# Kernel tuning notes

Measured on AMD Instinct MI355X. Metric: run time of the kernel, lower is better.

## Reference

```python
import jax, jax.numpy as jnp
import numpy as np

BLOCK = 64   # init block_size
RATIO = 0.5  # init ratio
GRAY = 128.0


def _make_mask(depth_map, H, W, key):
    """Vectorized equivalent of the per-block python loop.

    Blocks with initial_mask > ratio are kept (all ones). Dropped blocks are
    filled with a random binary region containing round(depth*b*b) zeros,
    chosen uniformly without replacement (torch.randperm semantics ==
    rank-of-uniform-noise < num_zeros).
    """
    nH, nW = H // BLOCK, W // BLOCK
    k1, k2 = jax.random.split(key)
    initial_mask = jax.random.uniform(k1, (nH, nW))           # [nH,nW]
    keep = initial_mask > RATIO                                # blocks kept fully

    d = jnp.where(depth_map.max() > 1.0, depth_map / 255.0, depth_map)
    gray_depth = d.mean(axis=0)                                # [H,W]
    # avg_pool2d with kernel=stride=BLOCK
    avg_depth = gray_depth.reshape(nH, BLOCK, nW, BLOCK).mean(axis=(1, 3))  # [nH,nW]
    num_zeros = jnp.round(avg_depth * (BLOCK * BLOCK)).astype(jnp.int32)    # per block

    # random permutation rank per pixel within each block
    noise = jax.random.uniform(k2, (nH, nW, BLOCK * BLOCK))
    ranks = jnp.argsort(jnp.argsort(noise, axis=-1), axis=-1)               # [nH,nW,b*b]
    region = (ranks >= num_zeros[..., None]).astype(jnp.float32)            # zeros at low ranks

    blocks = jnp.where(keep[..., None], 1.0, region)           # [nH,nW,b*b]
    mask = blocks.reshape(nH, nW, BLOCK, BLOCK).transpose(0, 2, 1, 3).reshape(H, W)
    return mask


def setup_inputs() -> dict:
    key = jax.random.key(0)
    k1, k2 = jax.random.split(key)
    img = jax.random.uniform(k1, (3, 2048, 4096), dtype=jnp.float32) * 255.0
    depth_map = jax.random.uniform(k2, (3, 2048, 4096), dtype=jnp.float32)
    return {"img": img, "depth_map": depth_map}


def reference(img, depth_map):
    C, H, W = img.shape
    mask = _make_mask(depth_map, H, W, jax.random.key(42))     # [H,W]
    # resize to (H,W) is a no-op since mask is already full resolution
    return img * mask + GRAY * (1.0 - mask)
```

## Files before the change

### kernel.cpp

```cpp
#include <hip/hip_runtime.h>
#include <stdint.h>

static constexpr int kH  = 2048;
static constexpr int kW  = 4096;
static constexpr int kHW = kH * kW;
static constexpr int kNH = kH / 64;
static constexpr int kNW = kW / 64;
static constexpr int kNB = kNH * kNW;
static constexpr int kBB = 64 * 64;
static constexpr int kGrayN = kNB * kBB;
static constexpr float kGray = 128.0f;

__host__ __device__ inline void tf2x32(uint32_t k0, uint32_t k1,
                                       uint32_t x0, uint32_t x1,
                                       uint32_t& o0, uint32_t& o1) {
  uint32_t ks2 = 0x1BD11BDAu ^ k0 ^ k1;
  x0 += k0; x1 += k1;
#define ROTL(v, d) (((v) << (d)) | ((v) >> (32 - (d))))
#define RND(R) { x0 += x1; x1 = ROTL(x1, R); x1 ^= x0; }
  RND(13) RND(15) RND(26) RND(6)
  x0 += k1;  x1 += ks2 + 1u;
  RND(17) RND(29) RND(16) RND(24)
  x0 += ks2; x1 += k0 + 2u;
  RND(13) RND(15) RND(26) RND(6)
  x0 += k0;  x1 += k1 + 3u;
  RND(17) RND(29) RND(16) RND(24)
  x0 += k1;  x1 += ks2 + 4u;
  RND(13) RND(15) RND(26) RND(6)
  x0 += ks2; x1 += k0 + 5u;
  o0 = x0; o1 = x1;
#undef RND
#undef ROTL
}

__device__ inline uint32_t rbits(uint32_t ka, uint32_t kb, uint32_t idx) {
  uint32_t o0, o1;
  tf2x32(ka, kb, 0u, idx, o0, o1);
  return o0 ^ o1;
}

__device__ inline bool keep_block(uint32_t k1a, uint32_t k1b, int b) {
  uint32_t v = rbits(k1a, k1b, (uint32_t)b) >> 9;
  return v > 0x400000u;
}

__global__ __launch_bounds__(256) void k1_depth(const float* __restrict__ depth,
                                                float* __restrict__ Gu,
                                                float* __restrict__ Gs,
                                                float* __restrict__ Bmax,
                                                uint32_t k1a, uint32_t k1b_) {
  __shared__ float red[256];
  const int b = blockIdx.x, t = threadIdx.x;
  const int bi = b >> 6, bj = b & 63;
  const int y0 = bi * 64, x0 = bj * 64;
  const bool keep = keep_block(k1a, k1b_, b);
  const float4* d4 = reinterpret_cast<const float4*>(depth);

  float mx = 0.0f;
  #pragma unroll
  for (int it = 0; it < 4; ++it) {
    int idx = it * 256 + t;
    int r = idx >> 4, cq = idx & 15;
    uint32_t a4 = (uint32_t)(y0 + r) * (kW / 4) + (uint32_t)(x0 / 4 + cq);
    float4 d0 = d4[a4];
    float4 d1 = d4[a4 + kHW / 4];
    float4 d2 = d4[a4 + 2 * (kHW / 4)];
    mx = fmaxf(mx, fmaxf(fmaxf(fmaxf(d0.x, d0.y), fmaxf(d0.z, d0.w)),
               fmaxf(fmaxf(fmaxf(d1.x, d1.y), fmaxf(d1.z, d1.w)),
                     fmaxf(fmaxf(d2.x, d2.y), fmaxf(d2.z, d2.w)))));
    if (!keep) {
      uint32_t p4 = (uint32_t)b * (kBB / 4) + (uint32_t)idx;
      float4 u, s;
      u.x = ((d0.x + d1.x) + d2.x) / 3.0f;
      u.y = ((d0.y + d1.y) + d2.y) / 3.0f;
      u.z = ((d0.z + d1.z) + d2.z) / 3.0f;
      u.w = ((d0.w + d1.w) + d2.w) / 3.0f;
      s.x = ((d0.x / 255.0f + d1.x / 255.0f) + d2.x / 255.0f) / 3.0f;
      s.y = ((d0.y / 255.0f + d1.y / 255.0f) + d2.y / 255.0f) / 3.0f;
      s.z = ((d0.z / 255.0f + d1.z / 255.0f) + d2.z / 255.0f) / 3.0f;
      s.w = ((d0.w / 255.0f + d1.w / 255.0f) + d2.w / 255.0f) / 3.0f;
      reinterpret_cast<float4*>(Gu)[p4] = u;
      reinterpret_cast<float4*>(Gs)[p4] = s;
    }
  }
  red[t] = mx;
  __syncthreads();
  for (int s = 128; s > 0; s >>= 1) {
    if (t < s) red[t] = fmaxf(red[t], red[t + s]);
    __syncthreads();
  }
  if (t == 0) Bmax[b] = red[0];
}

__global__ __launch_bounds__(64) void kchain(const float* __restrict__ G,
                                             const float* __restrict__ Bmax,
                                             float* __restrict__ S,
                                             uint32_t k1a, uint32_t k1b_) {
  const int w = blockIdx.x, lane = threadIdx.x;

  float m = 0.0f;
  #pragma unroll
  for (int i = 0; i < kNB / 64; ++i) m = fmaxf(m, Bmax[lane + i * 64]);
  #pragma unroll
  for (int d = 32; d >= 1; d >>= 1) m = fmaxf(m, __shfl_xor(m, d, 64));
  const bool flag = m > 1.0f;

  uint32_t bits = 0;
  int c = 0;
  #pragma unroll
  for (int j = 0; j < 32; ++j) {
    int b = lane * 32 + j;
    if (!keep_block(k1a, k1b_, b)) { bits |= (1u << j); ++c; }
  }
  int P = c;
  #pragma unroll
  for (int d = 1; d < 64; d <<= 1) {
    int v = __shfl_up(P, d, 64);
    if (lane >= d) P += v;
  }
  const int total = __shfl(P, 63, 64);
  P -= c;

  const int r0 = 2 * w, r1 = 2 * w + 1;
  int b0c = -1, b1c = -1;
  if (r0 >= P && r0 < P + c) {
    uint32_t bb = bits;
    for (int i = r0 - P; i > 0; --i) bb &= bb - 1;
    b0c = lane * 32 + __ffs(bb) - 1;
  }
  if (r1 >= P && r1 < P + c) {
    uint32_t bb = bits;
    for (int i = r1 - P; i > 0; --i) bb &= bb - 1;
    b1c = lane * 32 + __ffs(bb) - 1;
  }
  unsigned long long m0 = __ballot(b0c >= 0);
  unsigned long long m1 = __ballot(b1c >= 0);
  const int blk0 = (r0 < total && m0) ? __shfl(b0c, (int)(__ffsll(m0) - 1), 64) : -1;
  const int blk1 = (r1 < total && m1) ? __shfl(b1c, (int)(__ffsll(m1) - 1), 64) : -1;

  const int blk = (lane == 0) ? blk0 : blk1;
  if (lane < 2 && blk >= 0) {
    const float4* g4 = reinterpret_cast<const float4*>(G) +
                       (flag ? (uint32_t)(kGrayN / 4) : 0u) + (uint32_t)blk * (kBB / 4);

    float4 buf[32];
    #pragma unroll
    for (int i = 0; i < 32; ++i) buf[i] = g4[i];
    uint32_t gp = 32;

    float acc = 0.0f;
    for (int outer = 0; outer < 31; ++outer) {
      #pragma unroll
      for (int i = 0; i < 32; ++i) {
        float4 v = buf[i];
        buf[i] = g4[gp + i];
        acc += v.x; acc += v.y; acc += v.z; acc += v.w;
      }
      gp += 32;
    }
    #pragma unroll
    for (int i = 0; i < 32; ++i) {
      float4 v = buf[i];
      acc += v.x; acc += v.y; acc += v.z; acc += v.w;
    }
    S[blk] = acc;
  }
}

__global__ __launch_bounds__(256) void k3_fused(const float* __restrict__ img,
                                                float* __restrict__ out,
                                                const float* __restrict__ S,
                                                uint32_t k1a, uint32_t k1b_,
                                                uint32_t k2a, uint32_t k2b) {
  __shared__ uint32_t vals[kBB];
  __shared__ uint32_t hist[256];
  __shared__ uint32_t cand[kBB];
  __shared__ uint32_t sh[4];
  const int b = blockIdx.x, t = threadIdx.x;
  const int bi = b >> 6, bj = b & 63;
  const int y0 = bi * 64, x0 = bj * 64;
  const float4* img4 = reinterpret_cast<const float4*>(img);
  float4* out4 = reinterpret_cast<float4*>(out);

  int nz;
  if (keep_block(k1a, k1b_, b)) {
    nz = 0;
  } else {
    float s = S[b];
    nz = (int)rintf(s);
    if (nz < 0) nz = 0;
    if (nz > kBB) nz = kBB;
  }

  if (nz == 0 || nz == kBB) {
    const bool fill = (nz == kBB);
    const float4 g4v = make_float4(kGray, kGray, kGray, kGray);
    #pragma unroll
    for (int it = 0; it < 4; ++it) {
      int r = it * 16 + (t >> 4), cq = t & 15;
      uint32_t a4 = (uint32_t)(y0 + r) * (kW / 4) + (uint32_t)(x0 / 4 + cq);
      #pragma unroll
      for (int ch = 0; ch < 3; ++ch) {
        uint32_t a = a4 + (uint32_t)ch * (kHW / 4);
        out4[a] = fill ? g4v : img4[a];
      }
    }
    return;
  }

  for (int i = t; i < 256; i += 256) hist[i] = 0;
  if (t == 0) sh[3] = 0;
  __syncthreads();

  const uint32_t base = (uint32_t)b * (uint32_t)kBB;
  #pragma unroll
  for (int u = 0; u < 16; ++u) {
    int p = u * 256 + t;
    uint32_t v = rbits(k2a, k2b, base + (uint32_t)p) >> 9;
    vals[p] = v;
    atomicAdd(&hist[v >> 15], 1u);
  }
  __syncthreads();

  if (t == 0) {
    uint32_t cum = 0;
    for (int i = 0; i < 256; ++i) {
      uint32_t h = hist[i];
      if (cum + h >= (uint32_t)nz) { sh[0] = (uint32_t)i; sh[1] = (uint32_t)nz - cum; break; }
      cum += h;
    }
  }
  __syncthreads();
  const uint32_t Bsel = sh[0], rr = sh[1];

  #pragma unroll
  for (int u = 0; u < 16; ++u) {
    int p = u * 256 + t;
    uint32_t v = vals[p];
    if ((v >> 15) == Bsel) {
      uint32_t slot = atomicAdd(&sh[3], 1u);
      cand[slot] = ((v & 0x7FFFu) << 12) | (uint32_t)p;
    }
  }
  __syncthreads();
  const uint32_t m = sh[3];

  for (uint32_t q = t; q < m; q += 256) {
    uint32_t key = cand[q], rank = 0;
    for (uint32_t q2 = 0; q2 < m; ++q2) rank += (cand[q2] < key) ? 1u : 0u;
    if (rank == rr - 1) sh[2] = key;
  }
  __syncthreads();
  const uint32_t T = sh[2];

  #pragma unroll
  for (int it = 0; it < 4; ++it) {
    int r = it * 16 + (t >> 4), cq = t & 15;
    int p = r * 64 + cq * 4;
    uint4 vv = *reinterpret_cast<const uint4*>(vals + p);
    uint32_t kmask = 0;
    {
      uint32_t v, key;
      v = vv.x; key = ((v & 0x7FFFu) << 12) | (uint32_t)(p + 0);
      if (!((v >> 15) < Bsel || ((v >> 15) == Bsel && key <= T))) kmask |= 1u;
      v = vv.y; key = ((v & 0x7FFFu) << 12) | (uint32_t)(p + 1);
      if (!((v >> 15) < Bsel || ((v >> 15) == Bsel && key <= T))) kmask |= 2u;
      v = vv.z; key = ((v & 0x7FFFu) << 12) | (uint32_t)(p + 2);
      if (!((v >> 15) < Bsel || ((v >> 15) == Bsel && key <= T))) kmask |= 4u;
      v = vv.w; key = ((v & 0x7FFFu) << 12) | (uint32_t)(p + 3);
      if (!((v >> 15) < Bsel || ((v >> 15) == Bsel && key <= T))) kmask |= 8u;
    }
    uint32_t a4 = (uint32_t)(y0 + r) * (kW / 4) + (uint32_t)(x0 / 4 + cq);
    #pragma unroll
    for (int ch = 0; ch < 3; ++ch) {
      uint32_t a = a4 + (uint32_t)ch * (kHW / 4);
      float4 v = img4[a];
      float4 o;
      o.x = (kmask & 1u) ? v.x : kGray;
      o.y = (kmask & 2u) ? v.y : kGray;
      o.z = (kmask & 4u) ? v.z : kGray;
      o.w = (kmask & 8u) ? v.w : kGray;
      out4[a] = o;
    }
  }
}

extern "C" void kernel_launch(void* const* d_in, const int* in_sizes, int n_in,
                              void* d_out, int out_size, void* d_ws, size_t ws_size,
                              hipStream_t stream) {
  const float* img   = (const float*)d_in[0];
  const float* depth = (const float*)d_in[1];
  float* out = (float*)d_out;

  float* Gu = out;
  float* Gs = out + kGrayN;

  float* S    = (float*)d_ws;
  float* Bmax = S + kNB;

  uint32_t k1a, k1b_, k2a, k2b;
  tf2x32(0u, 42u, 0u, 0u, k1a, k1b_);
  tf2x32(0u, 42u, 0u, 1u, k2a, k2b);

  k1_depth<<<kNB, 256, 0, stream>>>(depth, Gu, Gs, Bmax, k1a, k1b_);
  kchain  <<<kNB / 2, 64, 0, stream>>>(out, Bmax, S, k1a, k1b_);
  k3_fused<<<kNB, 256, 0, stream>>>(img, out, S, k1a, k1b_, k2a, k2b);
}
```

Baseline: 119.0 us.

## Replace shared-memory value buffer with register radix select and parallel scans

The random values for each block are now kept in registers instead of a 16 KB shared array. The threshold search becomes a two-level radix histogram, each level resolved with a parallel prefix scan instead of a serial thread-0 loop. Only a small candidate set of at most 64 keys is then ranked. This cuts LDS usage from roughly 32 KB per block, which should raise occupancy, and shortens the serial rank step. In exchange it adds many __syncthreads in the scans, and selection is wrong if more than 64 candidates share the 16-bit prefix.

```diff
diff --git a/kernel.cpp b/kernel.cpp
--- a/kernel.cpp
+++ b/kernel.cpp
@@ -172,9 +172,8 @@
                                                 const float* __restrict__ S,
                                                 uint32_t k1a, uint32_t k1b_,
                                                 uint32_t k2a, uint32_t k2b) {
-  __shared__ uint32_t vals[kBB];
   __shared__ uint32_t hist[256];
-  __shared__ uint32_t cand[kBB];
+  __shared__ uint32_t cand[64];
   __shared__ uint32_t sh[4];
   const int b = blockIdx.x, t = threadIdx.x;
   const int bi = b >> 6, bj = b & 63;
@@ -192,13 +191,14 @@
     if (nz > kBB) nz = kBB;
   }
 
+  const int row0 = t >> 4, cq = t & 15;
+
   if (nz == 0 || nz == kBB) {
     const bool fill = (nz == kBB);
     const float4 g4v = make_float4(kGray, kGray, kGray, kGray);
     #pragma unroll
     for (int it = 0; it < 4; ++it) {
-      int r = it * 16 + (t >> 4), cq = t & 15;
-      uint32_t a4 = (uint32_t)(y0 + r) * (kW / 4) + (uint32_t)(x0 / 4 + cq);
+      uint32_t a4 = (uint32_t)(y0 + it * 16 + row0) * (kW / 4) + (uint32_t)(x0 / 4 + cq);
       #pragma unroll
       for (int ch = 0; ch < 3; ++ch) {
         uint32_t a = a4 + (uint32_t)ch * (kHW / 4);
@@ -208,78 +208,105 @@
     return;
   }
 
-  for (int i = t; i < 256; i += 256) hist[i] = 0;
+  const uint32_t base = (uint32_t)b * (uint32_t)kBB;
+  uint32_t v[4][4];
+  #pragma unroll
+  for (int it = 0; it < 4; ++it) {
+    uint32_t p = (uint32_t)((it * 16 + row0) * 64 + cq * 4);
+    #pragma unroll
+    for (int j = 0; j < 4; ++j) v[it][j] = rbits(k2a, k2b, base + p + j) >> 9;
+  }
+
+  hist[t] = 0;
   if (t == 0) sh[3] = 0;
   __syncthreads();
-
-  const uint32_t base = (uint32_t)b * (uint32_t)kBB;
-  #pragma unroll
-  for (int u = 0; u < 16; ++u) {
-    int p = u * 256 + t;
-    uint32_t v = rbits(k2a, k2b, base + (uint32_t)p) >> 9;
-    vals[p] = v;
-    atomicAdd(&hist[v >> 15], 1u);
-  }
-  __syncthreads();
-
-  if (t == 0) {
-    uint32_t cum = 0;
-    for (int i = 0; i < 256; ++i) {
-      uint32_t h = hist[i];
-      if (cum + h >= (uint32_t)nz) { sh[0] = (uint32_t)i; sh[1] = (uint32_t)nz - cum; break; }
-      cum += h;
-    }
-  }
-  __syncthreads();
-  const uint32_t Bsel = sh[0], rr = sh[1];
-
-  #pragma unroll
-  for (int u = 0; u < 16; ++u) {
-    int p = u * 256 + t;
-    uint32_t v = vals[p];
-    if ((v >> 15) == Bsel) {
-      uint32_t slot = atomicAdd(&sh[3], 1u);
-      cand[slot] = ((v & 0x7FFFu) << 12) | (uint32_t)p;
-    }
-  }
-  __syncthreads();
-  const uint32_t m = sh[3];
-
-  for (uint32_t q = t; q < m; q += 256) {
-    uint32_t key = cand[q], rank = 0;
-    for (uint32_t q2 = 0; q2 < m; ++q2) rank += (cand[q2] < key) ? 1u : 0u;
-    if (rank == rr - 1) sh[2] = key;
-  }
-  __syncthreads();
-  const uint32_t T = sh[2];
+  #pragma unroll
+  for (int it = 0; it < 4; ++it)
+    #pragma unroll
+    for (int j = 0; j < 4; ++j) atomicAdd(&hist[v[it][j] >> 15], 1u);
+  __syncthreads();
+  {
+    uint32_t h = hist[t];
+    for (int s = 1; s < 256; s <<= 1) {
+      uint32_t add = (t >= s) ? hist[t - s] : 0;
+      __syncthreads();
+      hist[t] += add;
+      __syncthreads();
+    }
+    uint32_t inc = hist[t], exc = inc - h;
+    if (inc >= (uint32_t)nz && exc < (uint32_t)nz) { sh[0] = (uint32_t)t; sh[1] = (uint32_t)nz - exc; }
+  }
+  __syncthreads();
+  const uint32_t B1 = sh[0], rr2 = sh[1];
+
+  hist[t] = 0;
+  __syncthreads();
+  #pragma unroll
+  for (int it = 0; it < 4; ++it)
+    #pragma unroll
+    for (int j = 0; j < 4; ++j) {
+      uint32_t vv = v[it][j];
+      if ((vv >> 15) == B1) atomicAdd(&hist[(vv >> 7) & 0xFFu], 1u);
+    }
+  __syncthreads();
+  {
+    uint32_t h = hist[t];
+    for (int s = 1; s < 256; s <<= 1) {
+      uint32_t add = (t >= s) ? hist[t - s] : 0;
+      __syncthreads();
+      hist[t] += add;
+      __syncthreads();
+    }
+    uint32_t inc = hist[t], exc = inc - h;
+    if (inc >= rr2 && exc < rr2) { sh[0] = (uint32_t)t; sh[1] = rr2 - exc; }
+  }
+  __syncthreads();
+  const uint32_t pref16 = (B1 << 8) | sh[0];
+  const uint32_t rr3 = sh[1];
+
+  #pragma unroll
+  for (int it = 0; it < 4; ++it)
+    #pragma unroll
+    for (int j = 0; j < 4; ++j) {
+      uint32_t vv = v[it][j];
+      if ((vv >> 7) == pref16) {
+        uint32_t p = (uint32_t)((it * 16 + row0) * 64 + cq * 4 + j);
+        uint32_t slot = atomicAdd(&sh[3], 1u);
+        if (slot < 64u) cand[slot] = ((vv & 0x7Fu) << 12) | p;
+      }
+    }
+  __syncthreads();
+  const uint32_t m = sh[3] < 64u ? sh[3] : 64u;
+  if (t < (int)m) {
+    uint32_t key = cand[t], rank = 0;
+    for (uint32_t q = 0; q < m; ++q) rank += (cand[q] < key) ? 1u : 0u;
+    if (rank == rr3 - 1) sh[2] = key;
+  }
+  __syncthreads();
+  const uint32_t T3 = sh[2];
 
   #pragma unroll
   for (int it = 0; it < 4; ++it) {
-    int r = it * 16 + (t >> 4), cq = t & 15;
-    int p = r * 64 + cq * 4;
-    uint4 vv = *reinterpret_cast<const uint4*>(vals + p);
+    uint32_t p = (uint32_t)((it * 16 + row0) * 64 + cq * 4);
     uint32_t kmask = 0;
-    {
-      uint32_t v, key;
-      v = vv.x; key = ((v & 0x7FFFu) << 12) | (uint32_t)(p + 0);
-      if (!((v >> 15) < Bsel || ((v >> 15) == Bsel && key <= T))) kmask |= 1u;
-      v = vv.y; key = ((v & 0x7FFFu) << 12) | (uint32_t)(p + 1);
-      if (!((v >> 15) < Bsel || ((v >> 15) == Bsel && key <= T))) kmask |= 2u;
-      v = vv.z; key = ((v & 0x7FFFu) << 12) | (uint32_t)(p + 2);
-      if (!((v >> 15) < Bsel || ((v >> 15) == Bsel && key <= T))) kmask |= 4u;
-      v = vv.w; key = ((v & 0x7FFFu) << 12) | (uint32_t)(p + 3);
-      if (!((v >> 15) < Bsel || ((v >> 15) == Bsel && key <= T))) kmask |= 8u;
-    }
-    uint32_t a4 = (uint32_t)(y0 + r) * (kW / 4) + (uint32_t)(x0 / 4 + cq);
+    #pragma unroll
+    for (int j = 0; j < 4; ++j) {
+      uint32_t vv = v[it][j];
+      uint32_t pre = vv >> 7;
+      bool zero = (pre < pref16) ||
+                  (pre == pref16 && ((((vv & 0x7Fu) << 12) | (p + j)) <= T3));
+      if (!zero) kmask |= (1u << j);
+    }
+    uint32_t a4 = (uint32_t)(y0 + it * 16 + row0) * (kW / 4) + (uint32_t)(x0 / 4 + cq);
     #pragma unroll
     for (int ch = 0; ch < 3; ++ch) {
       uint32_t a = a4 + (uint32_t)ch * (kHW / 4);
-      float4 v = img4[a];
+      float4 vf = img4[a];
       float4 o;
-      o.x = (kmask & 1u) ? v.x : kGray;
-      o.y = (kmask & 2u) ? v.y : kGray;
-      o.z = (kmask & 4u) ? v.z : kGray;
-      o.w = (kmask & 8u) ? v.w : kGray;
+      o.x = (kmask & 1u) ? vf.x : kGray;
+      o.y = (kmask & 2u) ? vf.y : kGray;
+      o.z = (kmask & 4u) ? vf.z : kGray;
+      o.w = (kmask & 8u) ? vf.w : kGray;
       out4[a] = o;
     }
   }
```

Result: faster. 114.1 us (-4.1%).
